# Optimization experiments

Hardware: AMD Instinct MI355X
Metric: run time of the kernel (lower is better)

## Reference

```python
import jax, jax.numpy as jnp
import numpy as np

B, D, H = 512, 512, 512
EPS = 1e-12  # torch F.normalize eps


def _l2norm(x):
    n = jnp.sqrt(jnp.sum(x * x, axis=1, keepdims=True))
    return x / jnp.maximum(n, EPS)


def setup_inputs() -> dict:
    key = jax.random.key(0)
    k1, k2, k3, k4 = jax.random.split(key, 4)
    scale1 = 1.0 / np.sqrt(D * D)  # roughly torch Linear init scale
    scale2 = 1.0 / np.sqrt(H)
    return {
        "image_embeds": jax.random.normal(k1, (B, D), dtype=jnp.float32),
        "text_embeds": jax.random.normal(k2, (B, D), dtype=jnp.float32),
        "W1": jax.random.normal(k3, (D * D, H), dtype=jnp.float32) * scale1,
        "b1": jnp.zeros((H,), dtype=jnp.float32),
        "W2": jax.random.normal(k4, (H, 1), dtype=jnp.float32) * scale2,
        "b2": jnp.zeros((1,), dtype=jnp.float32),
    }


def reference(image_embeds, text_embeds, W1, b1, W2, b2):
    img = _l2norm(image_embeds)  # [B, D]
    txt = _l2norm(text_embeds)  # [B, D]
    # Flattened outer product img_i * txt_j hits W1 row i*D + j, so reshape
    # W1 to [D, D, H] and contract as a per-sample bilinear form --
    # mathematically identical to flatten(bmm) @ W1 but never materializes
    # the [B, D*D] intermediate.
    W1r = W1.reshape(D, D, H)
    tmp = jnp.einsum('ijh,bj->bih', W1r, txt)       # [B, D, H]
    h = jnp.einsum('bi,bih->bh', img, tmp) + b1     # [B, H]
    h = jax.nn.relu(h)
    # Dropout is identity in eval mode.
    logits = h @ W2 + b2                            # [B, 1]
    return logits
```

## Files before the change

### kernel.cpp

```cpp
#include <hip/hip_runtime.h>
#include <hip/hip_bf16.h>


typedef float f4 __attribute__((ext_vector_type(4)));
typedef short bf8v __attribute__((ext_vector_type(8)));
typedef unsigned short u16;
typedef unsigned int u32;

#define DD 512
#define NT 8
#define BN 64
#define SPLITK 32
#define ISTR 16
#define NJW 16
#define NSTEP 256
#define W1LD 40
#define TXLD 40

__device__ __forceinline__ u16 f2bf(float f) {
  __hip_bfloat16 h = __float2bfloat16(f);
  union { __hip_bfloat16 h; u16 u; } c; c.h = h; return c.u;
}
__device__ __forceinline__ float lo_bf(u32 d) { return __uint_as_float(d << 16); }
__device__ __forceinline__ float hi_bf(u32 d) { return __uint_as_float(d & 0xffff0000u); }

__global__ __launch_bounds__(256) void ccpc_norm(
    const float* __restrict__ img, const float* __restrict__ txt,
    u16* __restrict__ imgn_t, u16* __restrict__ txtn) {
  int b = blockIdx.x & 511;
  bool is_txt = blockIdx.x >= 512;
  const float* src = (is_txt ? txt : img) + (size_t)b * DD;
  int t = threadIdx.x;
  float x0 = src[t], x1 = src[t + 256];
  float ss = x0 * x0 + x1 * x1;
  #pragma unroll
  for (int o = 32; o > 0; o >>= 1) ss += __shfl_down(ss, o);
  __shared__ float wsum[4];
  if ((t & 63) == 0) wsum[t >> 6] = ss;
  __syncthreads();
  float tot = wsum[0] + wsum[1] + wsum[2] + wsum[3];
  float sc = 1.0f / fmaxf(sqrtf(tot), 1e-12f);
  u16 u0 = f2bf(x0 * sc), u1 = f2bf(x1 * sc);
  if (!is_txt) {
    imgn_t[(size_t)t * DD + b] = u0;
    imgn_t[(size_t)(t + 256) * DD + b] = u1;
  } else {
    txtn[(size_t)b * DD + t] = u0;
    txtn[(size_t)b * DD + t + 256] = u1;
  }
}

__global__ __launch_bounds__(512, 2) void ccpc_gemm(
    const float* __restrict__ W1, const u16* __restrict__ imgn_t,
    const u16* __restrict__ txtn, float* __restrict__ part) {
  __shared__ u16 lds_w1[3 * 64 * W1LD];
  __shared__ u16 lds_tx[512 * TXLD];

  const int tid = threadIdx.x;
  const int bid = blockIdx.x;
  const int nt = bid & (NT - 1), sp = bid >> 3;
  const int n0 = nt * BN;
  const int i0 = sp * ISTR;
  const int wv = tid >> 6, l = tid & 63, l15 = l & 15, l4 = l >> 4;

  const int scol = tid & 63;
  const int srow = (tid >> 6) * 4;
  const int gcol = n0 + scol;

  f4 acc[4][4];
  #pragma unroll
  for (int a = 0; a < 4; ++a)
    #pragma unroll
    for (int c = 0; c < 4; ++c) acc[a][c] = {0.f, 0.f, 0.f, 0.f};

  float buf0[4], buf1[4], buf2[4], buf3[4];
  int4 treg0, treg1, treg2, treg3;
  u32 tpk[4][4];

  auto issueW1 = [&](int t, float (&ld)[4]) {
    int rb = (i0 + (t & (ISTR - 1))) * DD + (t >> 4) * 32 + srow;
    const float* p = W1 + (size_t)rb * DD + gcol;
    ld[0] = p[0]; ld[1] = p[DD]; ld[2] = p[2 * DD]; ld[3] = p[3 * DD];
  };
  auto writeW1 = [&](int t, float (&ld)[4]) {
    u32 d0 = ((u32)f2bf(ld[1]) << 16) | f2bf(ld[0]);
    u32 d1 = ((u32)f2bf(ld[3]) << 16) | f2bf(ld[2]);
    u16* dst = lds_w1 + (t % 3) * (64 * W1LD) + scol * W1LD + srow;
    *reinterpret_cast<uint2*>(dst) = make_uint2(d0, d1);
  };
  auto issueTX = [&](int jw) {
    const int4* p = reinterpret_cast<const int4*>(txtn + (size_t)tid * DD + jw * 32);
    treg0 = p[0]; treg1 = p[1]; treg2 = p[2]; treg3 = p[3];
  };
  auto writeTX = [&]() {
    int4* dst = reinterpret_cast<int4*>(lds_tx + (size_t)tid * TXLD);
    dst[0] = treg0; dst[1] = treg1; dst[2] = treg2; dst[3] = treg3;
  };
  auto readTX = [&]() {
    #pragma unroll
    for (int m = 0; m < 4; ++m) {
      const uint4* p = reinterpret_cast<const uint4*>(
          lds_tx + (wv * 64 + m * 16 + l15) * TXLD + l4 * 8);
      uint4 v = *p;
      tpk[m][0] = v.x; tpk[m][1] = v.y; tpk[m][2] = v.z; tpk[m][3] = v.w;
    }
  };

  auto compute = [&](int t) {
    const int i = t & (ISTR - 1);
    bf8v bfr[4];
    const u16* wb = lds_w1 + (t % 3) * (64 * W1LD);
    #pragma unroll
    for (int fn = 0; fn < 4; ++fn) {
      const uint4* p = reinterpret_cast<const uint4*>(wb + (fn * 16 + l15) * W1LD + l4 * 8);
      uint4 v = *p;
      union { u32 u[4]; bf8v v8; } cb;
      cb.u[0] = v.x; cb.u[1] = v.y; cb.u[2] = v.z; cb.u[3] = v.w;
      bfr[fn] = cb.v8;
    }
    const int irow = (i0 + i) * DD + wv * 64 + l15;
    float im[4];
    im[0] = __uint_as_float(((u32)imgn_t[irow]) << 16);
    im[1] = __uint_as_float(((u32)imgn_t[irow + 16]) << 16);
    im[2] = __uint_as_float(((u32)imgn_t[irow + 32]) << 16);
    im[3] = __uint_as_float(((u32)imgn_t[irow + 48]) << 16);
    #pragma unroll
    for (int m = 0; m < 4; ++m) {
      union { u32 u[4]; bf8v v8; } ca;
      #pragma unroll
      for (int d = 0; d < 4; ++d) {
        float p0 = lo_bf(tpk[m][d]) * im[m];
        float p1 = hi_bf(tpk[m][d]) * im[m];
        ca.u[d] = ((u32)f2bf(p1) << 16) | f2bf(p0);
      }
      #pragma unroll
      for (int fn = 0; fn < 4; ++fn)
        acc[m][fn] = __builtin_amdgcn_mfma_f32_16x16x32_bf16(ca.v8, bfr[fn], acc[m][fn], 0, 0, 0);
    }
  };

  auto stepBar = [&]() {
    asm volatile("s_waitcnt lgkmcnt(0)" ::: "memory");
    __builtin_amdgcn_s_barrier();
  };

  auto body = [&](int t, float (&ldI)[4], float (&ldC)[4]) {
    if ((t & (ISTR - 1)) == 0) readTX();
    if (t + 3 < NSTEP) issueW1(t + 3, ldI);
    if ((t & (ISTR - 1)) == 4 && (t >> 4) + 1 < NJW) issueTX((t >> 4) + 1);
    compute(t);
    if (t + 1 < NSTEP) writeW1(t + 1, ldC);
    if ((t & (ISTR - 1)) == (ISTR - 1) && t + 1 < NSTEP) writeTX();
    stepBar();
  };

  issueW1(0, buf0);
  issueW1(1, buf1);
  issueW1(2, buf2);
  issueTX(0);
  writeW1(0, buf0);
  writeTX();
  stepBar();

  for (int t = 0; t < NSTEP; t += 4) {
    body(t + 0, buf3, buf1);
    body(t + 1, buf0, buf2);
    body(t + 2, buf1, buf3);
    body(t + 3, buf2, buf0);
  }

  float* pout = part + (size_t)sp * (512 * 512);
  #pragma unroll
  for (int m = 0; m < 4; ++m) {
    #pragma unroll
    for (int fn = 0; fn < 4; ++fn) {
      int brow = wv * 64 + m * 16 + l4 * 4;
      int hcol = n0 + fn * 16 + l15;
      #pragma unroll
      for (int r = 0; r < 4; ++r)
        pout[(size_t)(brow + r) * 512 + hcol] = acc[m][fn][r];
    }
  }
}

__global__ __launch_bounds__(512) void ccpc_fin(
    const float* __restrict__ part, const float* __restrict__ b1,
    const float* __restrict__ w2, const float* __restrict__ b2,
    float* __restrict__ out) {
  int b = blockIdx.x, h = threadIdx.x;
  const float* p = part + (size_t)b * 512 + h;
  float s = 0.f;
  #pragma unroll
  for (int sp = 0; sp < SPLITK; ++sp) s += p[(size_t)sp * (512 * 512)];
  float hv = fmaxf(s + b1[h], 0.f) * w2[h];
  #pragma unroll
  for (int o = 32; o > 0; o >>= 1) hv += __shfl_down(hv, o);
  __shared__ float red[8];
  if ((h & 63) == 0) red[h >> 6] = hv;
  __syncthreads();
  if (h == 0) {
    float r = 0.f;
    #pragma unroll
    for (int w = 0; w < 8; ++w) r += red[w];
    out[b] = r + b2[0];
  }
}

extern "C" void kernel_launch(void* const* d_in, const int* in_sizes, int n_in,
                              void* d_out, int out_size, void* d_ws, size_t ws_size,
                              hipStream_t stream) {
  const float* img = (const float*)d_in[0];
  const float* txt = (const float*)d_in[1];
  const float* W1  = (const float*)d_in[2];
  const float* b1  = (const float*)d_in[3];
  const float* W2  = (const float*)d_in[4];
  const float* b2  = (const float*)d_in[5];
  float* out = (float*)d_out;

  char* ws = (char*)d_ws;
  u16* imgn_t = (u16*)ws;
  u16* txtn   = (u16*)(ws + 524288);
  float* part = (float*)(ws + 1048576);

  ccpc_norm<<<1024, 256, 0, stream>>>(img, txt, imgn_t, txtn);
  ccpc_gemm<<<256, 512, 0, stream>>>(W1, imgn_t, txtn, part);
  ccpc_fin<<<512, 512, 0, stream>>>(part, b1, W2, b2, out);
}
```

Baseline: 857.7 us.

## Double split-K blocks, drop LDS text staging, stage image rows in LDS

Doubles the split-K factor to 64 so the GEMM launches 512 blocks of 8 image rows each, and raises the occupancy hint to 4 blocks per CU. The large LDS text buffer is removed: text fragments now load straight from global memory into registers, and the block's image rows are staged once into a small LDS array. Float-to-bf16 packing switches to the v_cvt_pk_bf16_f32 instruction. In exchange the partial-sum buffer and the finalize reduction double in size, and the direct global text loads are no longer prefetched ahead of use.

```diff
diff --git a/kernel.cpp b/kernel.cpp
--- a/kernel.cpp
+++ b/kernel.cpp
@@ -10,13 +10,17 @@
 #define DD 512
 #define NT 8
 #define BN 64
-#define SPLITK 32
-#define ISTR 16
+#define SPLITK 64
+#define ISTR 8
 #define NJW 16
-#define NSTEP 256
+#define NSTEP 128
 #define W1LD 40
-#define TXLD 40
-
+
+__device__ __forceinline__ u32 cvtpk(float lo, float hi) {
+  u32 r;
+  asm("v_cvt_pk_bf16_f32 %0, %1, %2" : "=v"(r) : "v"(lo), "v"(hi));
+  return r;
+}
 __device__ __forceinline__ u16 f2bf(float f) {
   __hip_bfloat16 h = __float2bfloat16(f);
   union { __hip_bfloat16 h; u16 u; } c; c.h = h; return c.u;
@@ -50,11 +54,11 @@
   }
 }
 
-__global__ __launch_bounds__(512, 2) void ccpc_gemm(
+__global__ __launch_bounds__(512, 4) void ccpc_gemm(
     const float* __restrict__ W1, const u16* __restrict__ imgn_t,
     const u16* __restrict__ txtn, float* __restrict__ part) {
   __shared__ u16 lds_w1[3 * 64 * W1LD];
-  __shared__ u16 lds_tx[512 * TXLD];
+  __shared__ u16 lds_im[ISTR * DD];
 
   const int tid = threadIdx.x;
   const int bid = blockIdx.x;
@@ -64,9 +68,16 @@
   const int wv = tid >> 6, l = tid & 63, l15 = l & 15, l4 = l >> 4;
 
   const int scol = tid & 63;
-  const int srow = (tid >> 6) * 4;
+  const int srow = wv * 4;
   const int gcol = n0 + scol;
 
+  {
+    const uint4* ip = reinterpret_cast<const uint4*>(
+        imgn_t + (size_t)(i0 + wv) * DD + scol * 8);
+    uint4 iv = *ip;
+    *reinterpret_cast<uint4*>(lds_im + wv * DD + scol * 8) = iv;
+  }
+
   f4 acc[4][4];
   #pragma unroll
   for (int a = 0; a < 4; ++a)
@@ -74,40 +85,30 @@
     for (int c = 0; c < 4; ++c) acc[a][c] = {0.f, 0.f, 0.f, 0.f};
 
   float buf0[4], buf1[4], buf2[4], buf3[4];
-  int4 treg0, treg1, treg2, treg3;
   u32 tpk[4][4];
 
   auto issueW1 = [&](int t, float (&ld)[4]) {
-    int rb = (i0 + (t & (ISTR - 1))) * DD + (t >> 4) * 32 + srow;
+    int rb = (i0 + (t & (ISTR - 1))) * DD + (t >> 3) * 32 + srow;
     const float* p = W1 + (size_t)rb * DD + gcol;
     ld[0] = p[0]; ld[1] = p[DD]; ld[2] = p[2 * DD]; ld[3] = p[3 * DD];
   };
   auto writeW1 = [&](int t, float (&ld)[4]) {
-    u32 d0 = ((u32)f2bf(ld[1]) << 16) | f2bf(ld[0]);
-    u32 d1 = ((u32)f2bf(ld[3]) << 16) | f2bf(ld[2]);
+    u32 d0 = cvtpk(ld[0], ld[1]);
+    u32 d1 = cvtpk(ld[2], ld[3]);
     u16* dst = lds_w1 + (t % 3) * (64 * W1LD) + scol * W1LD + srow;
     *reinterpret_cast<uint2*>(dst) = make_uint2(d0, d1);
   };
-  auto issueTX = [&](int jw) {
-    const int4* p = reinterpret_cast<const int4*>(txtn + (size_t)tid * DD + jw * 32);
-    treg0 = p[0]; treg1 = p[1]; treg2 = p[2]; treg3 = p[3];
-  };
-  auto writeTX = [&]() {
-    int4* dst = reinterpret_cast<int4*>(lds_tx + (size_t)tid * TXLD);
-    dst[0] = treg0; dst[1] = treg1; dst[2] = treg2; dst[3] = treg3;
-  };
-  auto readTX = [&]() {
+  auto loadTX = [&](int w) {
     #pragma unroll
     for (int m = 0; m < 4; ++m) {
       const uint4* p = reinterpret_cast<const uint4*>(
-          lds_tx + (wv * 64 + m * 16 + l15) * TXLD + l4 * 8);
+          txtn + (size_t)(wv * 64 + m * 16 + l15) * DD + w * 32 + l4 * 8);
       uint4 v = *p;
       tpk[m][0] = v.x; tpk[m][1] = v.y; tpk[m][2] = v.z; tpk[m][3] = v.w;
     }
   };
 
   auto compute = [&](int t) {
-    const int i = t & (ISTR - 1);
     bf8v bfr[4];
     const u16* wb = lds_w1 + (t % 3) * (64 * W1LD);
     #pragma unroll
@@ -118,12 +119,12 @@
       cb.u[0] = v.x; cb.u[1] = v.y; cb.u[2] = v.z; cb.u[3] = v.w;
       bfr[fn] = cb.v8;
     }
-    const int irow = (i0 + i) * DD + wv * 64 + l15;
+    const int ib = (t & (ISTR - 1)) * DD + wv * 64 + l15;
     float im[4];
-    im[0] = __uint_as_float(((u32)imgn_t[irow]) << 16);
-    im[1] = __uint_as_float(((u32)imgn_t[irow + 16]) << 16);
-    im[2] = __uint_as_float(((u32)imgn_t[irow + 32]) << 16);
-    im[3] = __uint_as_float(((u32)imgn_t[irow + 48]) << 16);
+    im[0] = __uint_as_float(((u32)lds_im[ib]) << 16);
+    im[1] = __uint_as_float(((u32)lds_im[ib + 16]) << 16);
+    im[2] = __uint_as_float(((u32)lds_im[ib + 32]) << 16);
+    im[3] = __uint_as_float(((u32)lds_im[ib + 48]) << 16);
     #pragma unroll
     for (int m = 0; m < 4; ++m) {
       union { u32 u[4]; bf8v v8; } ca;
@@ -131,7 +132,7 @@
       for (int d = 0; d < 4; ++d) {
         float p0 = lo_bf(tpk[m][d]) * im[m];
         float p1 = hi_bf(tpk[m][d]) * im[m];
-        ca.u[d] = ((u32)f2bf(p1) << 16) | f2bf(p0);
+        ca.u[d] = cvtpk(p0, p1);
       }
       #pragma unroll
       for (int fn = 0; fn < 4; ++fn)
@@ -145,21 +146,17 @@
   };
 
   auto body = [&](int t, float (&ldI)[4], float (&ldC)[4]) {
-    if ((t & (ISTR - 1)) == 0) readTX();
+    if ((t & (ISTR - 1)) == 0) loadTX(t >> 3);
     if (t + 3 < NSTEP) issueW1(t + 3, ldI);
-    if ((t & (ISTR - 1)) == 4 && (t >> 4) + 1 < NJW) issueTX((t >> 4) + 1);
     compute(t);
     if (t + 1 < NSTEP) writeW1(t + 1, ldC);
-    if ((t & (ISTR - 1)) == (ISTR - 1) && t + 1 < NSTEP) writeTX();
     stepBar();
   };
 
   issueW1(0, buf0);
   issueW1(1, buf1);
   issueW1(2, buf2);
-  issueTX(0);
   writeW1(0, buf0);
-  writeTX();
   stepBar();
 
   for (int t = 0; t < NSTEP; t += 4) {
@@ -190,7 +187,7 @@
   int b = blockIdx.x, h = threadIdx.x;
   const float* p = part + (size_t)b * 512 + h;
   float s = 0.f;
-  #pragma unroll
+  #pragma unroll 16
   for (int sp = 0; sp < SPLITK; ++sp) s += p[(size_t)sp * (512 * 512)];
   float hv = fmaxf(s + b1[h], 0.f) * w2[h];
   #pragma unroll
@@ -223,6 +220,6 @@
   float* part = (float*)(ws + 1048576);
 
   ccpc_norm<<<1024, 256, 0, stream>>>(img, txt, imgn_t, txtn);
-  ccpc_gemm<<<256, 512, 0, stream>>>(W1, imgn_t, txtn, part);
+  ccpc_gemm<<<512, 512, 0, stream>>>(W1, imgn_t, txtn, part);
   ccpc_fin<<<512, 512, 0, stream>>>(part, b1, W2, b2, out);
 }
```

After: 1.122 ms. +30.8%, slower.
